# Performance work log

Hardware: AMD Instinct MI355X
Metric: run time of the kernel (lower is better)

Reference implementation:

```python
import jax, jax.numpy as jnp
import numpy as np

NUM_CLASSES = 17
NUM_ENSEMBLE = 10
TAU = 10.0
TOP_K = 20  # min(self.k=20, filter_K=200)
EPS = 1e-12


def _l2norm(x, axis=-1):
    # matches F.normalize: x / max(||x||, 1e-12)
    n = jnp.sqrt(jnp.sum(x * x, axis=axis, keepdims=True))
    return x / jnp.maximum(n, EPS)


def _batch_ensemble(x, weight, alpha_be, gamma_be, ensemble_bias):
    # x: [M, D1] -> [E, M, D2]  (BatchEnsemble.forward, kept in [E, M, D2] layout)
    r = x[None, :, :] * alpha_be[:, None, :]              # [E, M, D1]
    w = jnp.einsum('emd,od->emo', r, weight)              # [E, M, D2]
    return w * gamma_be[:, None, :] + ensemble_bias[:, None, :]


def _compute_logits(z, supports, labels, weight, alpha_be, gamma_be, ensemble_bias):
    mlp_z = _batch_ensemble(z, weight, alpha_be, gamma_be, ensemble_bias)         # [E, B, D2]
    mlp_s = _batch_ensemble(supports, weight, alpha_be, gamma_be, ensemble_bias)  # [E, N, D2]
    lbl = labels / (jnp.sum(labels, axis=0, keepdims=True) + EPS)                 # [N, C]
    centroids = jnp.einsum('nc,end->ecd', lbl, mlp_s)                             # [E, C, D2]
    zn = _l2norm(mlp_z)
    cn = _l2norm(centroids)
    return TAU * jnp.einsum('ebd,ecd->ebc', zn, cn)                               # [E, B, C]


def _cosine_distance(X, Y):
    Xn = _l2norm(X, axis=1)
    Yn = _l2norm(Y, axis=1)
    XX = jnp.sum(Xn * Xn, axis=1)[:, None]   # [B, 1]
    YY = jnp.sum(Yn * Yn, axis=1)            # [N]
    XY = 2.0 * (Xn @ Yn.T)                   # [B, N]
    return XX + YY - XY


def _target_generation(z, supports, labels, weight, alpha_be, gamma_be, ensemble_bias):
    dist = _cosine_distance(z, supports)      # [B, N]
    W = jnp.exp(-dist)
    B = W.shape[0]
    _, idx = jax.lax.top_k(W, TOP_K)                                   # [B, K]
    mask = jnp.zeros_like(W).at[jnp.arange(B)[:, None], idx].set(1.0)  # [B, N]
    temp = _compute_logits(supports, supports, labels, weight, alpha_be, gamma_be, ensemble_bias)  # [E, N, C]
    tgt_oh = jax.nn.one_hot(jnp.argmax(temp, axis=-1), NUM_CLASSES, dtype=temp.dtype)  # [E, N, C]
    soft = jax.nn.softmax(temp, axis=-1)
    targets = jnp.einsum('bn,enc->ebc', mask, tgt_oh)
    targets = targets / (jnp.sum(targets, axis=2, keepdims=True) + EPS)
    outputs = jnp.einsum('bn,enc->ebc', mask, soft)
    outputs = outputs / (jnp.sum(outputs, axis=2, keepdims=True) + EPS)
    outputs = jnp.mean(outputs, axis=0)   # [B, C]
    return targets, outputs


def setup_inputs() -> dict:
    key = jax.random.key(0)
    ks = jax.random.split(key, 7)
    B, N, D1, D2, E, C = 4096, 3400, 2048, 1024, NUM_ENSEMBLE, NUM_CLASSES
    z = jax.random.normal(ks[0], (B, D1), dtype=jnp.float32)
    supports = jax.random.normal(ks[1], (N, D1), dtype=jnp.float32)
    y = jax.random.randint(ks[2], (N,), 0, C)
    labels = jax.nn.one_hot(y, C, dtype=jnp.float32)
    weight = jax.random.normal(ks[3], (D2, D1), dtype=jnp.float32) * 0.02
    alpha_be = 1.0 + 0.1 * jax.random.normal(ks[4], (E, D1), dtype=jnp.float32)
    gamma_be = 1.0 + 0.1 * jax.random.normal(ks[5], (E, D2), dtype=jnp.float32)
    ensemble_bias = jnp.zeros((E, D2), dtype=jnp.float32)
    return {"z": z, "supports": supports, "labels": labels, "weight": weight,
            "alpha_be": alpha_be, "gamma_be": gamma_be, "ensemble_bias": ensemble_bias}


def reference(z, supports, labels, weight, alpha_be, gamma_be, ensemble_bias):
    targets, outputs = _target_generation(z, supports, labels, weight, alpha_be, gamma_be, ensemble_bias)
    logits = _compute_logits(z, supports, labels, weight, alpha_be, gamma_be, ensemble_bias)  # [E, B, C]
    return outputs, logits
```

## Files before the change

kernel.cpp:

```cpp
#include <hip/hip_runtime.h>
#include <math.h>

#define B_    4096
#define N_    3400
#define NP_   3456
#define NP2_  3584
#define D1_   2048
#define D2_   1024
#define E_    10
#define NE_   (E_ * D2_)
#define NDOT_ 256
#define NEX_  (NE_ + NDOT_)
#define ZOFF_ 3456
#define MR_   7680
#define EC_   170
#define C_    17
#define TOPK_ 20
#define TAU_  10.0f

typedef __bf16 bf16x8 __attribute__((ext_vector_type(8)));
typedef __bf16 bf16x4 __attribute__((ext_vector_type(4)));
typedef float  f32x4  __attribute__((ext_vector_type(4)));

#define MFMA_(a,b,c) __builtin_amdgcn_mfma_f32_16x16x32_bf16(a,b,c,0,0,0)

__device__ inline float wsum64(float v){
  #pragma unroll
  for (int m = 1; m < 64; m <<= 1) v += __shfl_xor(v, m);
  return v;
}

__device__ __forceinline__ void gload_lds16(const unsigned short* g, unsigned short* l){
  __builtin_amdgcn_global_load_lds(
      (const __attribute__((address_space(1))) void*)g,
      (__attribute__((address_space(3))) void*)l, 16, 0, 0);
}

__global__ __launch_bounds__(256)
void prep_rows(const float* __restrict__ X, unsigned short* __restrict__ hi,
               unsigned short* __restrict__ lo, float* __restrict__ rinv){
  const int r = blockIdx.x, t = threadIdx.x;
  const float4* x4 = reinterpret_cast<const float4*>(X + (long)r * D1_);
  bf16x4* h4 = reinterpret_cast<bf16x4*>(hi + (long)r * D1_);
  bf16x4* l4 = reinterpret_cast<bf16x4*>(lo + (long)r * D1_);
  float ss = 0.f;
  #pragma unroll
  for (int it = 0; it < 2; ++it){
    int i = t + it * 256;
    float4 v = x4[i];
    float f[4] = {v.x, v.y, v.z, v.w};
    bf16x4 h, l;
    #pragma unroll
    for (int j = 0; j < 4; ++j){
      ss += f[j] * f[j];
      __bf16 hb = (__bf16)f[j];
      h[j] = hb;
      l[j] = (__bf16)(f[j] - (float)hb);
    }
    h4[i] = h; l4[i] = l;
  }
  __shared__ float red[256];
  red[t] = ss; __syncthreads();
  for (int s = 128; s; s >>= 1){ if (t < s) red[t] += red[t + s]; __syncthreads(); }
  if (t == 0) rinv[r] = 1.f / fmaxf(sqrtf(red[0]), 1e-12f);
}

__global__ __launch_bounds__(256)
void zfill_all(uint4* p0, long n0, uint4* p1, long n1, uint4* p2, long n2,
               uint4* p3, long n3, uint4* p4, long n4, uint4* p5, long n5){
  long i = (long)blockIdx.x * 256 + threadIdx.x;
  uint4 zz = make_uint4(0,0,0,0);
  if (i < n0){ p0[i] = zz; return; } i -= n0;
  if (i < n1){ p1[i] = zz; return; } i -= n1;
  if (i < n2){ p2[i] = zz; return; } i -= n2;
  if (i < n3){ p3[i] = zz; return; } i -= n3;
  if (i < n4){ p4[i] = zz; return; } i -= n4;
  if (i < n5){ p5[i] = zz; }
}

__global__ __launch_bounds__(256)
void labelprep(const float* __restrict__ labels, int* __restrict__ y, float* __restrict__ cnt){
  int n = blockIdx.x * 256 + threadIdx.x;
  if (n >= N_) return;
  int c = 0;
  #pragma unroll
  for (int cc = 0; cc < C_; ++cc) if (labels[n * C_ + cc] > 0.5f) c = cc;
  y[n] = c;
  atomicAdd(&cnt[c], 1.0f);
}

__global__ __launch_bounds__(256)
void wfold(const float* __restrict__ W, const float* __restrict__ alpha,
           unsigned short* __restrict__ wbf){
  long i = (long)blockIdx.x * 256 + threadIdx.x;
  const long perE = (long)D2_ * D1_ / 4;
  int e = (int)(i / perE);
  long r = i - (long)e * perE;
  int k4 = (int)(r & (D1_/4 - 1));
  float4 wv = reinterpret_cast<const float4*>(W)[r];
  float4 av = reinterpret_cast<const float4*>(alpha + (long)e * D1_)[k4];
  bf16x4 o;
  o[0] = (__bf16)(wv.x * av.x);
  o[1] = (__bf16)(wv.y * av.y);
  o[2] = (__bf16)(wv.z * av.z);
  o[3] = (__bf16)(wv.w * av.w);
  reinterpret_cast<bf16x4*>(wbf)[i] = o;
}

__global__ __launch_bounds__(256)
void transposeW(const float* __restrict__ W, float* __restrict__ WT){
  __shared__ float tile[32][33];
  const int bx = blockIdx.x, by = blockIdx.y;
  const int tx = threadIdx.x & 31, ty = threadIdx.x >> 5;
  #pragma unroll
  for (int i = 0; i < 4; ++i)
    tile[ty + i*8][tx] = W[(long)(by*32 + ty + i*8) * D1_ + bx*32 + tx];
  __syncthreads();
  #pragma unroll
  for (int i = 0; i < 4; ++i)
    WT[(long)(bx*32 + ty + i*8) * D2_ + by*32 + tx] = tile[tx][ty + i*8];
}

__global__ __launch_bounds__(256)
void pbuild(const float* __restrict__ S, const int* __restrict__ y,
            const float* __restrict__ cnt, float* __restrict__ part){
  __shared__ float acc[C_ * 256];
  __shared__ float winv[C_];
  const int t = threadIdx.x, kb = blockIdx.x * 256, s = blockIdx.y;
  #pragma unroll
  for (int c = 0; c < C_; ++c) acc[c * 256 + t] = 0.f;
  if (t < C_) winv[t] = 1.f / (cnt[t] + 1e-12f);
  __syncthreads();
  const int n0 = s * 425, n1 = n0 + 425;
  for (int n = n0; n < n1; ++n){
    int c = y[n];
    acc[c * 256 + t] += winv[c] * S[(long)n * D1_ + kb + t];
  }
  #pragma unroll
  for (int c = 0; c < C_; ++c)
    part[((long)s * C_ + c) * D1_ + kb + t] = acc[c * 256 + t];
}

__global__ __launch_bounds__(256)
void pa2(const float* __restrict__ part, const float* __restrict__ alpha,
         float* __restrict__ A2){
  int i = blockIdx.x * 256 + threadIdx.x;
  if (i >= EC_ * D1_) return;
  int ec = i >> 11, k = i & (D1_ - 1);
  int e = ec / C_, c = ec - e * C_;
  float s = 0.f;
  #pragma unroll
  for (int kz = 0; kz < 8; ++kz) s += part[((long)kz * C_ + c) * D1_ + k];
  A2[i] = s * alpha[(long)e * D1_ + k];
}

__global__ __launch_bounds__(256)
void redcent(const float* __restrict__ part2, const float* __restrict__ gamma,
             const float* __restrict__ bias, const float* __restrict__ cnt,
             float* __restrict__ cent){
  int i = blockIdx.x * 256 + threadIdx.x;
  if (i >= EC_ * D2_) return;
  int ec = i >> 10, d = i & (D2_ - 1);
  int e = ec / C_, c = ec - e * C_;
  float s = 0.f;
  #pragma unroll
  for (int kz = 0; kz < 8; ++kz) s += part2[(long)kz * EC_ * D2_ + i];
  float sc = cnt[c] / (cnt[c] + 1e-12f);
  cent[i] = gamma[(long)e * D2_ + d] * s + bias[(long)e * D2_ + d] * sc;
}

__global__ __launch_bounds__(256)
void normgcn(float* __restrict__ cent, const float* __restrict__ gamma,
             const float* __restrict__ bias, float* __restrict__ gcn,
             float* __restrict__ bconst){
  const int ec = blockIdx.x, t = threadIdx.x;
  const int e = ec / C_;
  float4* c4 = reinterpret_cast<float4*>(cent + (long)ec * D2_);
  float4 v = c4[t];
  float ss = v.x*v.x + v.y*v.y + v.z*v.z + v.w*v.w;
  __shared__ float red[256];
  red[t] = ss; __syncthreads();
  for (int s = 128; s; s >>= 1){ if (t < s) red[t] += red[t + s]; __syncthreads(); }
  float rinv = 1.f / fmaxf(sqrtf(red[0]), 1e-12f);
  v.x *= rinv; v.y *= rinv; v.z *= rinv; v.w *= rinv;
  c4[t] = v;
  float4 g = reinterpret_cast<const float4*>(gamma + (long)e * D2_)[t];
  reinterpret_cast<float4*>(gcn + (long)ec * D2_)[t] =
      make_float4(g.x*v.x, g.y*v.y, g.z*v.z, g.w*v.w);
  float4 bb = reinterpret_cast<const float4*>(bias + (long)e * D2_)[t];
  float bs = bb.x*v.x + bb.y*v.y + bb.z*v.z + bb.w*v.w;
  __syncthreads();
  red[t] = bs; __syncthreads();
  for (int s = 128; s; s >>= 1){ if (t < s) red[t] += red[t + s]; __syncthreads(); }
  if (t == 0) bconst[ec] = red[0];
}

__global__ __launch_bounds__(256)
void redgb(const float* __restrict__ part2, const float* __restrict__ alpha,
           unsigned short* __restrict__ wbf){
  int i = blockIdx.x * 256 + threadIdx.x;
  if (i >= EC_ * D1_) return;
  int ec = i >> 11, k = i & (D1_ - 1);
  int e = ec / C_;
  float s = 0.f;
  #pragma unroll
  for (int kz = 0; kz < 8; ++kz) s += part2[(long)kz * EC_ * D1_ + i];
  __bf16 b = (__bf16)(alpha[(long)e * D1_ + k] * s);
  wbf[(long)(NE_ + ec) * D1_ + k] = *(unsigned short*)&b;
}

__global__ __launch_bounds__(256)
void gemm64k(const float* __restrict__ A, int lda,
             const float* __restrict__ Bm, int ldb,
             float* __restrict__ part, int M, int N, int KC)
{
  __shared__ float As[16][68];
  __shared__ float Bs[16][68];
  const int kz = blockIdx.z;
  const int m0 = blockIdx.y * 64, n0 = blockIdx.x * 64;
  const int t  = threadIdx.x;
  const int lr = t >> 2;
  const int lk = (t & 3) << 2;
  const int ty4 = (t >> 4) << 2;
  const int tx4 = (t & 15) << 2;
  const bool aok = (m0 + lr) < M;
  const bool bok = (n0 + lr) < N;
  const float* ap = A  + (long)(m0 + lr) * lda + lk;
  const float* bp = Bm + (long)(n0 + lr) * ldb + lk;
  float acc[4][4] = {{0.f}};
  const int k0b = kz * KC, k0e = k0b + KC;
  for (int k0 = k0b; k0 < k0e; k0 += 16){
    float4 av = make_float4(0,0,0,0), bv = make_float4(0,0,0,0);
    if (aok) av = *reinterpret_cast<const float4*>(ap + k0);
    if (bok) bv = *reinterpret_cast<const float4*>(bp + k0);
    As[lk+0][lr] = av.x; As[lk+1][lr] = av.y; As[lk+2][lr] = av.z; As[lk+3][lr] = av.w;
    Bs[lk+0][lr] = bv.x; Bs[lk+1][lr] = bv.y; Bs[lk+2][lr] = bv.z; Bs[lk+3][lr] = bv.w;
    __syncthreads();
    #pragma unroll
    for (int kk = 0; kk < 16; ++kk){
      float4 a = *reinterpret_cast<const float4*>(&As[kk][ty4]);
      float4 b = *reinterpret_cast<const float4*>(&Bs[kk][tx4]);
      float aa[4] = {a.x, a.y, a.z, a.w};
      float bb[4] = {b.x, b.y, b.z, b.w};
      #pragma unroll
      for (int i = 0; i < 4; ++i)
        #pragma unroll
        for (int j = 0; j < 4; ++j)
          acc[i][j] += aa[i] * bb[j];
    }
    __syncthreads();
  }
  float* Out = part + (long)kz * M * N;
  #pragma unroll
  for (int i = 0; i < 4; ++i){
    int m = m0 + ty4 + i;
    if (m >= M) continue;
    #pragma unroll
    for (int j = 0; j < 4; ++j){
      int n = n0 + tx4 + j;
      if (n >= N) continue;
      Out[(long)m * N + n] = acc[i][j];
    }
  }
}

__global__ __launch_bounds__(512)
void sc2(const unsigned short* __restrict__ zh, const unsigned short* __restrict__ zl,
         const unsigned short* __restrict__ sh, const unsigned short* __restrict__ sl,
         const float* __restrict__ zinv, const float* __restrict__ sinv,
         float* __restrict__ Out)
{
  __shared__ unsigned short LA[2][16384];
  __shared__ unsigned short LB[2][16384];
  const int n0 = blockIdx.x * 256;
  const int m0 = blockIdx.y * 256;
  const int t = threadIdx.x, lane = t & 63, w = t >> 6;
  const int wm = w >> 2, wn = w & 3;
  const int r15 = lane & 15, kb = lane >> 4;

  const long ao0 = (long)(m0 +       w*16 + r15) * D1_ + kb*8;
  const long ao1 = (long)(m0 + 128 + w*16 + r15) * D1_ + kb*8;
  const long bo0 = (long)(n0 +       w*16 + r15) * D1_ + kb*8;
  const long bo1 = (long)(n0 + 128 + w*16 + r15) * D1_ + kb*8;
  const unsigned d00 = (unsigned)(w*2)*512,     d01 = (unsigned)(w*2+1)*512;
  const unsigned d10 = (unsigned)((8+w)*2)*512, d11 = (unsigned)((8+w)*2+1)*512;
  const unsigned raB = (unsigned)wm*8192 + (unsigned)lane*8;
  const unsigned rbB = (unsigned)wn*4096 + (unsigned)lane*8;

#define STAGE_SC(buf, kt) do{ const int sg = (kt) >> 5; const int ko = ((kt) & 31)*64; \
    const unsigned short* ap = (sg == 2) ? zl : zh; \
    const unsigned short* bp = (sg == 1) ? sl : sh; \
    gload_lds16(ap+ao0+ko,    &LA[buf][d00]); gload_lds16(ap+ao0+ko+32, &LA[buf][d01]); \
    gload_lds16(ap+ao1+ko,    &LA[buf][d10]); gload_lds16(ap+ao1+ko+32, &LA[buf][d11]); \
    gload_lds16(bp+bo0+ko,    &LB[buf][d00]); gload_lds16(bp+bo0+ko+32, &LB[buf][d01]); \
    gload_lds16(bp+bo1+ko,    &LB[buf][d10]); gload_lds16(bp+bo1+ko+32, &LB[buf][d11]); }while(0)

  f32x4 acc[8][4];
  #pragma unroll
  for (int i = 0; i < 8; ++i)
    #pragma unroll
    for (int j = 0; j < 4; ++j)
      acc[i][j] = (f32x4){0.f, 0.f, 0.f, 0.f};

  STAGE_SC(0, 0);
  asm volatile("s_waitcnt vmcnt(0)" ::: "memory");
  __builtin_amdgcn_sched_barrier(0);
  __builtin_amdgcn_s_barrier();

  for (int kt = 0; kt < 96; ++kt){
    const int cb = kt & 1;
    if (kt < 95) STAGE_SC(cb ^ 1, kt + 1);

    bf16x8 ar[4][2], br[4][2];
    #pragma unroll
    for (int i = 0; i < 4; ++i){
      ar[i][0] = *(const bf16x8*)&LA[cb][raB + (unsigned)(i*2  )*512];
      ar[i][1] = *(const bf16x8*)&LA[cb][raB + (unsigned)(i*2+1)*512];
    }
    #pragma unroll
    for (int j = 0; j < 4; ++j){
      br[j][0] = *(const bf16x8*)&LB[cb][rbB + (unsigned)(j*2  )*512];
      br[j][1] = *(const bf16x8*)&LB[cb][rbB + (unsigned)(j*2+1)*512];
    }
    asm volatile("s_waitcnt lgkmcnt(0)" ::: "memory");
    __builtin_amdgcn_sched_barrier(0);
    __builtin_amdgcn_s_setprio(1);
    #pragma unroll
    for (int ks = 0; ks < 2; ++ks)
      #pragma unroll
      for (int i = 0; i < 4; ++i)
        #pragma unroll
        for (int j = 0; j < 4; ++j)
          acc[i][j] = MFMA_(ar[i][ks], br[j][ks], acc[i][j]);
    __builtin_amdgcn_s_setprio(0);
    #pragma unroll
    for (int i = 0; i < 4; ++i){
      ar[i][0] = *(const bf16x8*)&LA[cb][raB + (unsigned)((4+i)*2  )*512];
      ar[i][1] = *(const bf16x8*)&LA[cb][raB + (unsigned)((4+i)*2+1)*512];
    }
    asm volatile("s_waitcnt lgkmcnt(0)" ::: "memory");
    __builtin_amdgcn_sched_barrier(0);
    __builtin_amdgcn_s_setprio(1);
    #pragma unroll
    for (int ks = 0; ks < 2; ++ks)
      #pragma unroll
      for (int i = 0; i < 4; ++i)
        #pragma unroll
        for (int j = 0; j < 4; ++j)
          acc[4+i][j] = MFMA_(ar[i][ks], br[j][ks], acc[4+i][j]);
    __builtin_amdgcn_s_setprio(0);

    asm volatile("s_waitcnt vmcnt(0)" ::: "memory");
    __builtin_amdgcn_sched_barrier(0);
    __builtin_amdgcn_s_barrier();
  }
#undef STAGE_SC

  const int mb = m0 + wm * 128 + kb * 4;
  const int nc0 = n0 + wn * 64 + r15;
  #pragma unroll
  for (int j = 0; j < 4; ++j){
    int n = nc0 + j * 16;
    if (n >= N_) continue;
    float si = sinv[n];
    #pragma unroll
    for (int i = 0; i < 8; ++i)
      #pragma unroll
      for (int r = 0; r < 4; ++r){
        int m = mb + i*16 + r;
        Out[(long)m * N_ + n] = acc[i][j][r] * zinv[m] * si;
      }
  }
}

__global__ __launch_bounds__(512)
void nd2(const unsigned short* __restrict__ A,
         const unsigned short* __restrict__ Bw,
         const float* __restrict__ gamma,
         const float* __restrict__ bias,
         float* __restrict__ norm2,
         float* __restrict__ dots)
{
  __shared__ unsigned short LA[2][16384];
  __shared__ unsigned short LB[2][16384];
  const int n0 = blockIdx.x * 256;
  const int m0 = blockIdx.y * 256;
  const int t = threadIdx.x, lane = t & 63, w = t >> 6;
  const int wm = w >> 2, wn = w & 3;
  const int r15 = lane & 15, kb = lane >> 4;

  const unsigned short* a0p = A  + (long)(m0 +       w*16 + r15) * D1_ + kb*8;
  const unsigned short* a1p = A  + (long)(m0 + 128 + w*16 + r15) * D1_ + kb*8;
  const unsigned short* b0p = Bw + (long)(n0 +       w*16 + r15) * D1_ + kb*8;
  const unsigned short* b1p = Bw + (long)(n0 + 128 + w*16 + r15) * D1_ + kb*8;
  const unsigned d00 = (unsigned)(w*2)*512,     d01 = (unsigned)(w*2+1)*512;
  const unsigned d10 = (unsigned)((8+w)*2)*512, d11 = (unsigned)((8+w)*2+1)*512;
  const unsigned raB = (unsigned)wm*8192 + (unsigned)lane*8;
  const unsigned rbB = (unsigned)wn*4096 + (unsigned)lane*8;

#define STAGE_ND(buf, kt) do{ const int ko = (kt)*64; \
    gload_lds16(a0p+ko,    &LA[buf][d00]); gload_lds16(a0p+ko+32, &LA[buf][d01]); \
    gload_lds16(a1p+ko,    &LA[buf][d10]); gload_lds16(a1p+ko+32, &LA[buf][d11]); \
    gload_lds16(b0p+ko,    &LB[buf][d00]); gload_lds16(b0p+ko+32, &LB[buf][d01]); \
    gload_lds16(b1p+ko,    &LB[buf][d10]); gload_lds16(b1p+ko+32, &LB[buf][d11]); }while(0)

  f32x4 acc[8][4];
  #pragma unroll
  for (int i = 0; i < 8; ++i)
    #pragma unroll
    for (int j = 0; j < 4; ++j)
      acc[i][j] = (f32x4){0.f, 0.f, 0.f, 0.f};

  STAGE_ND(0, 0);
  asm volatile("s_waitcnt vmcnt(0)" ::: "memory");
  __builtin_amdgcn_sched_barrier(0);
  __builtin_amdgcn_s_barrier();

  for (int kt = 0; kt < 32; ++kt){
    const int cb = kt & 1;
    if (kt < 31) STAGE_ND(cb ^ 1, kt + 1);

    bf16x8 ar[4][2], br[4][2];
    #pragma unroll
    for (int i = 0; i < 4; ++i){
      ar[i][0] = *(const bf16x8*)&LA[cb][raB + (unsigned)(i*2  )*512];
      ar[i][1] = *(const bf16x8*)&LA[cb][raB + (unsigned)(i*2+1)*512];
    }
    #pragma unroll
    for (int j = 0; j < 4; ++j){
      br[j][0] = *(const bf16x8*)&LB[cb][rbB + (unsigned)(j*2  )*512];
      br[j][1] = *(const bf16x8*)&LB[cb][rbB + (unsigned)(j*2+1)*512];
    }
    asm volatile("s_waitcnt lgkmcnt(0)" ::: "memory");
    __builtin_amdgcn_sched_barrier(0);
    __builtin_amdgcn_s_setprio(1);
    #pragma unroll
    for (int ks = 0; ks < 2; ++ks)
      #pragma unroll
      for (int i = 0; i < 4; ++i)
        #pragma unroll
        for (int j = 0; j < 4; ++j)
          acc[i][j] = MFMA_(ar[i][ks], br[j][ks], acc[i][j]);
    __builtin_amdgcn_s_setprio(0);
    #pragma unroll
    for (int i = 0; i < 4; ++i){
      ar[i][0] = *(const bf16x8*)&LA[cb][raB + (unsigned)((4+i)*2  )*512];
      ar[i][1] = *(const bf16x8*)&LA[cb][raB + (unsigned)((4+i)*2+1)*512];
    }
    asm volatile("s_waitcnt lgkmcnt(0)" ::: "memory");
    __builtin_amdgcn_sched_barrier(0);
    __builtin_amdgcn_s_setprio(1);
    #pragma unroll
    for (int ks = 0; ks < 2; ++ks)
      #pragma unroll
      for (int i = 0; i < 4; ++i)
        #pragma unroll
        for (int j = 0; j < 4; ++j)
          acc[4+i][j] = MFMA_(ar[i][ks], br[j][ks], acc[4+i][j]);
    __builtin_amdgcn_s_setprio(0);

    asm volatile("s_waitcnt vmcnt(0)" ::: "memory");
    __builtin_amdgcn_sched_barrier(0);
    __builtin_amdgcn_s_barrier();
  }
#undef STAGE_ND

  if (n0 < NE_){
    const int e = n0 >> 10;
    float g4[4], b4[4];
    #pragma unroll
    for (int j = 0; j < 4; ++j){
      int n = n0 + wn * 64 + j * 16 + r15;
      g4[j] = gamma[n]; b4[j] = bias[n];
    }
    float rs[32];
    #pragma unroll
    for (int i = 0; i < 8; ++i)
      #pragma unroll
      for (int r = 0; r < 4; ++r){
        float s = 0.f;
        #pragma unroll
        for (int j = 0; j < 4; ++j){
          float v = acc[i][j][r] * g4[j] + b4[j];
          s += v * v;
        }
        rs[i*4 + r] = s;
      }
    #pragma unroll
    for (int msk = 1; msk < 16; msk <<= 1)
      #pragma unroll
      for (int q = 0; q < 32; ++q) rs[q] += __shfl_xor(rs[q], msk);
    float* red = (float*)&LA[0][0];
    if (r15 == 0){
      #pragma unroll
      for (int i = 0; i < 8; ++i)
        #pragma unroll
        for (int r = 0; r < 4; ++r)
          red[w * 128 + i*16 + kb*4 + r] = rs[i*4 + r];
    }
    __syncthreads();
    if (t < 256){
      int wmg = t >> 7;
      float v = 0.f;
      #pragma unroll
      for (int q = 0; q < 4; ++q)
        v += red[(wmg*4 + q) * 128 + (t & 127)];
      atomicAdd(&norm2[(long)(m0 + t) * E_ + e], v);
    }
  } else {
    const int dc0 = n0 - NE_ + wn * 64 + r15;
    const int mb = m0 + wm * 128 + kb * 4;
    #pragma unroll
    for (int j = 0; j < 4; ++j){
      int dc = dc0 + j * 16;
      #pragma unroll
      for (int i = 0; i < 8; ++i)
        #pragma unroll
        for (int r = 0; r < 4; ++r)
          dots[(long)(mb + i*16 + r) * NDOT_ + dc] = acc[i][j][r];
    }
  }
}

__global__ __launch_bounds__(256)
void topk20(const float* __restrict__ scores, int* __restrict__ idx){
  const int b = blockIdx.x, t = threadIdx.x;
  const int l = t & 63, wid = t >> 6;
  const float* row = scores + (long)b * N_;
  float v[14];
  #pragma unroll
  for (int j = 0; j < 14; ++j){
    int i = t + j * 256;
    v[j] = (i < N_) ? row[i] : -3.0e38f;
  }
  __shared__ float wv[4];
  __shared__ int   wi[4];
  for (int it = 0; it < TOPK_; ++it){
    float bv = -3.0e38f; int bj = 0;
    #pragma unroll
    for (int j = 0; j < 14; ++j)
      if (v[j] > bv){ bv = v[j]; bj = j; }
    int bi = t + bj * 256;
    #pragma unroll
    for (int m = 1; m < 64; m <<= 1){
      float ov = __shfl_xor(bv, m);
      int   oi = __shfl_xor(bi, m);
      if (ov > bv || (ov == bv && oi < bi)){ bv = ov; bi = oi; }
    }
    if (l == 0){ wv[wid] = bv; wi[wid] = bi; }
    __syncthreads();
    float gv = wv[0]; int gi = wi[0];
    #pragma unroll
    for (int k = 1; k < 4; ++k){
      float ov = wv[k]; int oi = wi[k];
      if (ov > gv || (ov == gv && oi < gi)){ gv = ov; gi = oi; }
    }
    if (t == 0) idx[b * TOPK_ + it] = gi;
    const int ot = gi & 255, oj = gi >> 8;
    #pragma unroll
    for (int j = 0; j < 14; ++j)
      if (t == ot && j == oj) v[j] = -3.0e38f;
    __syncthreads();
  }
}

__global__ __launch_bounds__(256)
void soft_build(const float* __restrict__ dots, const float* __restrict__ norm2,
                const float* __restrict__ bconst, float* __restrict__ soft){
  int id = blockIdx.x * 256 + threadIdx.x;
  if (id >= N_ * E_) return;
  int e = id % E_, n = id / E_;
  float rinv = 1.f / fmaxf(sqrtf(norm2[(long)n * E_ + e]), 1e-12f);
  float tv[C_];
  #pragma unroll
  for (int c = 0; c < C_; ++c)
    tv[c] = TAU_ * (dots[(long)n * NDOT_ + e*C_ + c] + bconst[e*C_ + c]) * rinv;
  float m = tv[0];
  #pragma unroll
  for (int c = 1; c < C_; ++c) m = fmaxf(m, tv[c]);
  float p[C_]; float sum = 0.f;
  #pragma unroll
  for (int c = 0; c < C_; ++c){ p[c] = expf(tv[c] - m); sum += p[c]; }
  float is = 1.f / sum;
  #pragma unroll
  for (int c = 0; c < C_; ++c)
    soft[((long)e * N_ + n) * C_ + c] = p[c] * is;
}

__global__ __launch_bounds__(256)
void logits_fin(const float* __restrict__ dots, const float* __restrict__ norm2,
                const float* __restrict__ bconst, float* __restrict__ out){
  int id = blockIdx.x * 256 + threadIdx.x;
  if (id >= B_ * E_) return;
  int e = id % E_, b = id / E_;
  int m = ZOFF_ + b;
  float rinv = 1.f / fmaxf(sqrtf(norm2[(long)m * E_ + e]), 1e-12f);
  float* op = out + (size_t)B_ * C_ + ((long)e * B_ + b) * C_;
  #pragma unroll
  for (int c = 0; c < C_; ++c)
    op[c] = TAU_ * (dots[(long)m * NDOT_ + e*C_ + c] + bconst[e*C_ + c]) * rinv;
}

__global__ __launch_bounds__(256)
void outputs_k(const float* __restrict__ soft, const int* __restrict__ idx, float* __restrict__ out){
  const int lane = threadIdx.x & 63;
  const int b = blockIdx.x * 4 + (threadIdx.x >> 6);
  const int* id = idx + b * TOPK_;
  float o = 0.f;
  for (int e = 0; e < E_; ++e){
    float S = 0.f;
    const float* se = soft + (long)e * N_ * C_;
    #pragma unroll
    for (int k = 0; k < TOPK_; ++k){
      int n = id[k];
      if (lane < C_) S += se[(long)n * C_ + lane];
    }
    float tot = wsum64(S);
    o += S / (tot + 1e-12f);
  }
  if (lane < C_) out[(long)b * C_ + lane] = o * (1.f / E_);
}

extern "C" void kernel_launch(void* const* d_in, const int* in_sizes, int n_in,
                              void* d_out, int out_size, void* d_ws, size_t ws_size,
                              hipStream_t stream){
  const float* z        = (const float*)d_in[0];
  const float* supports = (const float*)d_in[1];
  const float* labels   = (const float*)d_in[2];
  const float* weight   = (const float*)d_in[3];
  const float* alpha    = (const float*)d_in[4];
  const float* gamma    = (const float*)d_in[5];
  const float* bias     = (const float*)d_in[6];
  float* out = (float*)d_out;

  char* w = (char*)d_ws;
  size_t off = 0;
  auto alloc = [&](size_t bytes)->char*{
    char* p = w + off;
    off = (off + bytes + 255) & ~(size_t)255;
    return p;
  };

  float* zinv = (float*)alloc((size_t)B_ * 4);
  float* sinv = (float*)alloc((size_t)N_ * 4);
  float* cnt  = (float*)alloc((size_t)C_ * 4);
  int*   y    = (int*)  alloc((size_t)N_ * 4);
  int*   idx  = (int*)  alloc((size_t)B_ * TOPK_ * 4);
  unsigned short* SZ  = (unsigned short*)alloc((size_t)MR_ * D1_ * 2);
  unsigned short* zl  = (unsigned short*)alloc((size_t)B_  * D1_ * 2);
  unsigned short* sl  = (unsigned short*)alloc((size_t)NP_ * D1_ * 2);
  unsigned short* wbf = (unsigned short*)alloc((size_t)NEX_ * D1_ * 2);
  float* WT     = (float*)alloc((size_t)D1_ * D2_ * 4);
  float* part   = (float*)alloc((size_t)8 * C_ * D1_ * 4);
  float* A2     = (float*)alloc((size_t)EC_ * D1_ * 4);
  float* cent   = (float*)alloc((size_t)EC_ * D2_ * 4);
  float* gcn    = (float*)alloc((size_t)EC_ * D2_ * 4);
  float* bconst = (float*)alloc((size_t)256 * 4);
  float* scores = (float*)alloc((size_t)B_ * N_ * 4);
  float* dots   = (float*)alloc((size_t)MR_ * NDOT_ * 4);
  float* norm2  = (float*)alloc((size_t)MR_ * E_ * 4);
  float* soft   = (float*)alloc((size_t)E_ * N_ * C_ * 4);
  float* part2  = (float*)alloc((size_t)8 * EC_ * D1_ * 4);
  (void)ws_size; (void)in_sizes; (void)n_in; (void)out_size;

  unsigned short* sh = SZ;
  unsigned short* zh = SZ + (size_t)ZOFF_ * D1_;

  {
    long n0 = 14336, n1 = 14336, n2 = 32768, n3 = 22016, n4 = 19200, n5 = 5;
    long tot = n0 + n1 + n2 + n3 + n4 + n5;
    zfill_all<<<(int)((tot + 255) / 256), 256, 0, stream>>>(
        (uint4*)(sh + (size_t)N_ * D1_), n0,
        (uint4*)(sl + (size_t)N_ * D1_), n1,
        (uint4*)(SZ + (size_t)(ZOFF_ + B_) * D1_), n2,
        (uint4*)(wbf + (size_t)(NE_ + EC_) * D1_), n3,
        (uint4*)norm2, n4,
        (uint4*)cnt, n5);
  }
  labelprep<<<(N_ + 255) / 256, 256, 0, stream>>>(labels, y, cnt);

  prep_rows<<<B_, 256, 0, stream>>>(z, zh, zl, zinv);
  prep_rows<<<N_, 256, 0, stream>>>(supports, sh, sl, sinv);
  wfold<<<(int)((long)NE_ * D1_ / 4 / 256), 256, 0, stream>>>(weight, alpha, wbf);
  transposeW<<<dim3(D1_ / 32, D2_ / 32), 256, 0, stream>>>(weight, WT);

  sc2<<<dim3(NP2_ / 256, B_ / 256, 1), 512, 0, stream>>>(
      zh, zl, sh, sl, zinv, sinv, scores);
  topk20<<<B_, 256, 0, stream>>>(scores, idx);

  pbuild<<<dim3(D1_ / 256, 8), 256, 0, stream>>>(supports, y, cnt, part);
  pa2<<<(EC_ * D1_ + 255) / 256, 256, 0, stream>>>(part, alpha, A2);
  gemm64k<<<dim3(D2_ / 64, 3, 8), 256, 0, stream>>>(
      A2, D1_, weight, D1_, part2, EC_, D2_, 256);
  redcent<<<(EC_ * D2_ + 255) / 256, 256, 0, stream>>>(part2, gamma, bias, cnt, cent);
  normgcn<<<EC_, 256, 0, stream>>>(cent, gamma, bias, gcn, bconst);
  gemm64k<<<dim3(D1_ / 64, 3, 8), 256, 0, stream>>>(
      gcn, D2_, WT, D2_, part2, EC_, D1_, 128);
  redgb<<<(EC_ * D1_ + 255) / 256, 256, 0, stream>>>(part2, alpha, wbf);

  nd2<<<dim3(NEX_ / 256, MR_ / 256, 1), 512, 0, stream>>>(
      SZ, wbf, gamma, bias, norm2, dots);

  soft_build<<<(N_ * E_ + 255) / 256, 256, 0, stream>>>(dots, norm2, bconst, soft);
  outputs_k<<<B_ / 4, 256, 0, stream>>>(soft, idx, out);
  logits_fin<<<(B_ * E_ + 255) / 256, 256, 0, stream>>>(dots, norm2, bconst, out);
}
```

Before: 1.094 ms.

## Replace split-bf16 score GEMM with single bf16 pass plus fp32 rescoring of top candidates

The similarity GEMM now uses only the bf16 high parts of z and supports, so it does one K pass instead of three (hi*hi, hi*lo, lo*hi), and the low-part buffers and their writes are removed. To keep top-20 selection accurate, a top-32 candidate set is taken from the approximate scores and then rescored in fp32 against the original inputs before the final top-20 is picked. The risk is that a true top-20 neighbor falls outside the 32 bf16 candidates, and the extra top-k iterations and rescoring kernel add some cost.

```diff
diff --git a/kernel.cpp b/kernel.cpp
--- a/kernel.cpp
+++ b/kernel.cpp
@@ -3,7 +3,6 @@
 
 #define B_    4096
 #define N_    3400
-#define NP_   3456
 #define NP2_  3584
 #define D1_   2048
 #define D2_   1024
@@ -16,6 +15,7 @@
 #define EC_   170
 #define C_    17
 #define TOPK_ 20
+#define CAND_ 32
 #define TAU_  10.0f
 
 typedef __bf16 bf16x8 __attribute__((ext_vector_type(8)));
@@ -38,26 +38,23 @@
 
 __global__ __launch_bounds__(256)
 void prep_rows(const float* __restrict__ X, unsigned short* __restrict__ hi,
-               unsigned short* __restrict__ lo, float* __restrict__ rinv){
+               float* __restrict__ rinv){
   const int r = blockIdx.x, t = threadIdx.x;
   const float4* x4 = reinterpret_cast<const float4*>(X + (long)r * D1_);
   bf16x4* h4 = reinterpret_cast<bf16x4*>(hi + (long)r * D1_);
-  bf16x4* l4 = reinterpret_cast<bf16x4*>(lo + (long)r * D1_);
   float ss = 0.f;
   #pragma unroll
   for (int it = 0; it < 2; ++it){
     int i = t + it * 256;
     float4 v = x4[i];
     float f[4] = {v.x, v.y, v.z, v.w};
-    bf16x4 h, l;
+    bf16x4 h;
     #pragma unroll
     for (int j = 0; j < 4; ++j){
       ss += f[j] * f[j];
-      __bf16 hb = (__bf16)f[j];
-      h[j] = hb;
-      l[j] = (__bf16)(f[j] - (float)hb);
-    }
-    h4[i] = h; l4[i] = l;
+      h[j] = (__bf16)f[j];
+    }
+    h4[i] = h;
   }
   __shared__ float red[256];
   red[t] = ss; __syncthreads();
@@ -67,15 +64,14 @@
 
 __global__ __launch_bounds__(256)
 void zfill_all(uint4* p0, long n0, uint4* p1, long n1, uint4* p2, long n2,
-               uint4* p3, long n3, uint4* p4, long n4, uint4* p5, long n5){
+               uint4* p3, long n3, uint4* p4, long n4){
   long i = (long)blockIdx.x * 256 + threadIdx.x;
   uint4 zz = make_uint4(0,0,0,0);
   if (i < n0){ p0[i] = zz; return; } i -= n0;
   if (i < n1){ p1[i] = zz; return; } i -= n1;
   if (i < n2){ p2[i] = zz; return; } i -= n2;
   if (i < n3){ p3[i] = zz; return; } i -= n3;
-  if (i < n4){ p4[i] = zz; return; } i -= n4;
-  if (i < n5){ p5[i] = zz; }
+  if (i < n4){ p4[i] = zz; }
 }
 
 __global__ __launch_bounds__(256)
@@ -265,8 +261,7 @@
 }
 
 __global__ __launch_bounds__(512)
-void sc2(const unsigned short* __restrict__ zh, const unsigned short* __restrict__ zl,
-         const unsigned short* __restrict__ sh, const unsigned short* __restrict__ sl,
+void sc2(const unsigned short* __restrict__ zh, const unsigned short* __restrict__ sh,
          const float* __restrict__ zinv, const float* __restrict__ sinv,
          float* __restrict__ Out)
 {
@@ -278,22 +273,20 @@
   const int wm = w >> 2, wn = w & 3;
   const int r15 = lane & 15, kb = lane >> 4;
 
-  const long ao0 = (long)(m0 +       w*16 + r15) * D1_ + kb*8;
-  const long ao1 = (long)(m0 + 128 + w*16 + r15) * D1_ + kb*8;
-  const long bo0 = (long)(n0 +       w*16 + r15) * D1_ + kb*8;
-  const long bo1 = (long)(n0 + 128 + w*16 + r15) * D1_ + kb*8;
+  const unsigned short* a0p = zh + (long)(m0 +       w*16 + r15) * D1_ + kb*8;
+  const unsigned short* a1p = zh + (long)(m0 + 128 + w*16 + r15) * D1_ + kb*8;
+  const unsigned short* b0p = sh + (long)(n0 +       w*16 + r15) * D1_ + kb*8;
+  const unsigned short* b1p = sh + (long)(n0 + 128 + w*16 + r15) * D1_ + kb*8;
   const unsigned d00 = (unsigned)(w*2)*512,     d01 = (unsigned)(w*2+1)*512;
   const unsigned d10 = (unsigned)((8+w)*2)*512, d11 = (unsigned)((8+w)*2+1)*512;
   const unsigned raB = (unsigned)wm*8192 + (unsigned)lane*8;
   const unsigned rbB = (unsigned)wn*4096 + (unsigned)lane*8;
 
-#define STAGE_SC(buf, kt) do{ const int sg = (kt) >> 5; const int ko = ((kt) & 31)*64; \
-    const unsigned short* ap = (sg == 2) ? zl : zh; \
-    const unsigned short* bp = (sg == 1) ? sl : sh; \
-    gload_lds16(ap+ao0+ko,    &LA[buf][d00]); gload_lds16(ap+ao0+ko+32, &LA[buf][d01]); \
-    gload_lds16(ap+ao1+ko,    &LA[buf][d10]); gload_lds16(ap+ao1+ko+32, &LA[buf][d11]); \
-    gload_lds16(bp+bo0+ko,    &LB[buf][d00]); gload_lds16(bp+bo0+ko+32, &LB[buf][d01]); \
-    gload_lds16(bp+bo1+ko,    &LB[buf][d10]); gload_lds16(bp+bo1+ko+32, &LB[buf][d11]); }while(0)
+#define STAGE_SC(buf, kt) do{ const int ko = (kt)*64; \
+    gload_lds16(a0p+ko,    &LA[buf][d00]); gload_lds16(a0p+ko+32, &LA[buf][d01]); \
+    gload_lds16(a1p+ko,    &LA[buf][d10]); gload_lds16(a1p+ko+32, &LA[buf][d11]); \
+    gload_lds16(b0p+ko,    &LB[buf][d00]); gload_lds16(b0p+ko+32, &LB[buf][d01]); \
+    gload_lds16(b1p+ko,    &LB[buf][d10]); gload_lds16(b1p+ko+32, &LB[buf][d11]); }while(0)
 
   f32x4 acc[8][4];
   #pragma unroll
@@ -307,9 +300,9 @@
   __builtin_amdgcn_sched_barrier(0);
   __builtin_amdgcn_s_barrier();
 
-  for (int kt = 0; kt < 96; ++kt){
+  for (int kt = 0; kt < 32; ++kt){
     const int cb = kt & 1;
-    if (kt < 95) STAGE_SC(cb ^ 1, kt + 1);
+    if (kt < 31) STAGE_SC(cb ^ 1, kt + 1);
 
     bf16x8 ar[4][2], br[4][2];
     #pragma unroll
@@ -523,7 +516,7 @@
 }
 
 __global__ __launch_bounds__(256)
-void topk20(const float* __restrict__ scores, int* __restrict__ idx){
+void topk32(const float* __restrict__ scores, int* __restrict__ idx0){
   const int b = blockIdx.x, t = threadIdx.x;
   const int l = t & 63, wid = t >> 6;
   const float* row = scores + (long)b * N_;
@@ -535,7 +528,7 @@
   }
   __shared__ float wv[4];
   __shared__ int   wi[4];
-  for (int it = 0; it < TOPK_; ++it){
+  for (int it = 0; it < CAND_; ++it){
     float bv = -3.0e38f; int bj = 0;
     #pragma unroll
     for (int j = 0; j < 14; ++j)
@@ -555,12 +548,53 @@
       float ov = wv[k]; int oi = wi[k];
       if (ov > gv || (ov == gv && oi < gi)){ gv = ov; gi = oi; }
     }
-    if (t == 0) idx[b * TOPK_ + it] = gi;
+    if (t == 0) idx0[b * CAND_ + it] = gi;
     const int ot = gi & 255, oj = gi >> 8;
     #pragma unroll
     for (int j = 0; j < 14; ++j)
       if (t == ot && j == oj) v[j] = -3.0e38f;
     __syncthreads();
+  }
+}
+
+__global__ __launch_bounds__(256)
+void rescore20(const float* __restrict__ z, const float* __restrict__ S,
+               const int* __restrict__ idx0, const float* __restrict__ sinv,
+               int* __restrict__ idx){
+  const int b = blockIdx.x, t = threadIdx.x;
+  const int wv = t >> 6, l = t & 63;
+  __shared__ float sval[CAND_];
+  __shared__ int   sidx[CAND_];
+  const float4* zr = reinterpret_cast<const float4*>(z + (long)b * D1_);
+  for (int ci = wv; ci < CAND_; ci += 4){
+    int n = idx0[b * CAND_ + ci];
+    const float4* sr = reinterpret_cast<const float4*>(S + (long)n * D1_);
+    float p = 0.f;
+    #pragma unroll
+    for (int j = 0; j < 8; ++j){
+      float4 a = zr[l + j * 64];
+      float4 c = sr[l + j * 64];
+      p += a.x*c.x + a.y*c.y + a.z*c.z + a.w*c.w;
+    }
+    p = wsum64(p);
+    if (l == 0){ sval[ci] = p * sinv[n]; sidx[ci] = n; }
+  }
+  __syncthreads();
+  if (t < 64){
+    float v = (l < CAND_) ? sval[l] : -3.0e38f;
+    int   n = (l < CAND_) ? sidx[l] : 0x7fffffff;
+    for (int it = 0; it < TOPK_; ++it){
+      float bv = v; int bi = n, bl = l;
+      #pragma unroll
+      for (int m = 1; m < 64; m <<= 1){
+        float ov = __shfl_xor(bv, m);
+        int   oi = __shfl_xor(bi, m);
+        int   ol = __shfl_xor(bl, m);
+        if (ov > bv || (ov == bv && oi < bi)){ bv = ov; bi = oi; bl = ol; }
+      }
+      if (l == 0) idx[b * TOPK_ + it] = bi;
+      if (l == bl) v = -3.0e38f;
+    }
   }
 }
 
@@ -645,10 +679,9 @@
   float* sinv = (float*)alloc((size_t)N_ * 4);
   float* cnt  = (float*)alloc((size_t)C_ * 4);
   int*   y    = (int*)  alloc((size_t)N_ * 4);
+  int*   idx0 = (int*)  alloc((size_t)B_ * CAND_ * 4);
   int*   idx  = (int*)  alloc((size_t)B_ * TOPK_ * 4);
   unsigned short* SZ  = (unsigned short*)alloc((size_t)MR_ * D1_ * 2);
-  unsigned short* zl  = (unsigned short*)alloc((size_t)B_  * D1_ * 2);
-  unsigned short* sl  = (unsigned short*)alloc((size_t)NP_ * D1_ * 2);
   unsigned short* wbf = (unsigned short*)alloc((size_t)NEX_ * D1_ * 2);
   float* WT     = (float*)alloc((size_t)D1_ * D2_ * 4);
   float* part   = (float*)alloc((size_t)8 * C_ * D1_ * 4);
@@ -667,26 +700,26 @@
   unsigned short* zh = SZ + (size_t)ZOFF_ * D1_;
 
   {
-    long n0 = 14336, n1 = 14336, n2 = 32768, n3 = 22016, n4 = 19200, n5 = 5;
-    long tot = n0 + n1 + n2 + n3 + n4 + n5;
+    long n0 = 14336, n1 = 32768, n2 = 22016, n3 = 19200, n4 = 5;
+    long tot = n0 + n1 + n2 + n3 + n4;
     zfill_all<<<(int)((tot + 255) / 256), 256, 0, stream>>>(
         (uint4*)(sh + (size_t)N_ * D1_), n0,
-        (uint4*)(sl + (size_t)N_ * D1_), n1,
-        (uint4*)(SZ + (size_t)(ZOFF_ + B_) * D1_), n2,
-        (uint4*)(wbf + (size_t)(NE_ + EC_) * D1_), n3,
-        (uint4*)norm2, n4,
-        (uint4*)cnt, n5);
+        (uint4*)(SZ + (size_t)(ZOFF_ + B_) * D1_), n1,
+        (uint4*)(wbf + (size_t)(NE_ + EC_) * D1_), n2,
+        (uint4*)norm2, n3,
+        (uint4*)cnt, n4);
   }
   labelprep<<<(N_ + 255) / 256, 256, 0, stream>>>(labels, y, cnt);
 
-  prep_rows<<<B_, 256, 0, stream>>>(z, zh, zl, zinv);
-  prep_rows<<<N_, 256, 0, stream>>>(supports, sh, sl, sinv);
+  prep_rows<<<B_, 256, 0, stream>>>(z, zh, zinv);
+  prep_rows<<<N_, 256, 0, stream>>>(supports, sh, sinv);
   wfold<<<(int)((long)NE_ * D1_ / 4 / 256), 256, 0, stream>>>(weight, alpha, wbf);
   transposeW<<<dim3(D1_ / 32, D2_ / 32), 256, 0, stream>>>(weight, WT);
 
   sc2<<<dim3(NP2_ / 256, B_ / 256, 1), 512, 0, stream>>>(
-      zh, zl, sh, sl, zinv, sinv, scores);
-  topk20<<<B_, 256, 0, stream>>>(scores, idx);
+      zh, sh, zinv, sinv, scores);
+  topk32<<<B_, 256, 0, stream>>>(scores, idx0);
+  rescore20<<<B_, 256, 0, stream>>>(z, supports, idx0, sinv, idx);
 
   pbuild<<<dim3(D1_ / 256, 8), 256, 0, stream>>>(supports, y, cnt, part);
   pa2<<<(EC_ * D1_ + 255) / 256, 256, 0, stream>>>(part, alpha, A2);
```

Result: no change. 1.096 ms (+0.2%).
